# Kernel tuning notes

Hardware: AMD Instinct MI355X
Metric: run time of the kernel (lower is better)

Reference implementation:

```python
import jax, jax.numpy as jnp
import numpy as np

B, S = 8, 128
D_SENS, D_ACT, D_STR, D_ENC, DIM = 512, 32, 128, 128, 128
D_JOINT = D_STR + D_ENC  # 256


def _l2norm(x):
    return x / jnp.clip(jnp.linalg.norm(x, axis=-1, keepdims=True), 1e-12)


def _mlp(x, layers):
    # layers: list of (W, b); ReLU between layers, none on output
    n = len(layers)
    for i, (W, b) in enumerate(layers):
        x = x @ W + b
        if i < n - 1:
            x = jax.nn.relu(x)
    return x


def _meta_mlp(x, p):
    x = jax.nn.relu(x @ p['W1'] + p['b1'])
    x = jax.nn.relu(x @ p['W2'] + p['b2'])
    return x @ p['W3'] + p['b3']


def setup_inputs() -> dict:
    key = jax.random.key(0)
    it = iter(jax.random.split(key, 40))
    w = lambda shape, s=0.02: jax.random.normal(next(it), shape, jnp.float32) * s
    H = D_ACT * 4  # to_transitions hidden dim (default mlp_hidden_dim)
    return dict(
        sensory=jax.random.normal(next(it), (B, S, D_SENS), jnp.float32),
        actions=jax.random.normal(next(it), (B, S, D_ACT), jnp.float32),
        init_hidden=w((1, D_STR), 0.01),
        tW1=w((D_ACT, H)), tb1=w((H,)),
        tW2=w((H, H)), tb2=w((H,)),
        tW3=w((H, D_STR * D_STR)), tb3=w((D_STR * D_STR,)),
        enc_w=w((D_SENS, D_ENC)), enc_b=w((D_ENC,)),
        dec_w=w((D_ENC, D_SENS)), dec_b=w((D_SENS,)),
        q_w=w((D_JOINT, DIM)), k_w=w((D_JOINT, DIM)), v_w=w((D_JOINT, DIM)),
        mW1=w((DIM, 2 * DIM)), mb1=w((2 * DIM,)),
        mW2=w((2 * DIM, 2 * DIM)), mb2=w((2 * DIM,)),
        mW3=w((2 * DIM, DIM)), mb3=w((DIM,)),
        oW1=w((DIM, 2 * DIM)), ob1=w((2 * DIM,)),
        oW2=w((2 * DIM, 2 * DIM)), ob2=w((2 * DIM,)),
        oW3=w((2 * DIM, D_JOINT)), ob3=w((D_JOINT,)),
        sW1=w((2 * D_STR + 1, 2 * D_STR)), sb1=w((2 * D_STR,)),
        sW2=w((2 * D_STR, 2 * D_STR)), sb2=w((2 * D_STR,)),
        sW3=w((2 * D_STR, D_STR)), sb3=w((D_STR,)),
        integration_ratio=jnp.asarray(0.1, jnp.float32),
    )


def reference(sensory, actions, init_hidden, tW1, tb1, tW2, tb2, tW3, tb3,
              enc_w, enc_b, dec_w, dec_b, q_w, k_w, v_w,
              mW1, mb1, mW2, mb2, mW3, mb3,
              oW1, ob1, oW2, ob2, oW3, ob3,
              sW1, sb1, sW2, sb2, sW3, sb3, integration_ratio):
    mse = lambda a, b: jnp.mean((a - b) ** 2)

    # --- PathIntegration: actions -> transitions -> scripted RNN scan ---
    trans = _mlp(actions, [(tW1, tb1), (tW2, tb2), (tW3, tb3)])  # (B,S,ds*ds)
    trans = trans.reshape(B, S, D_STR, D_STR)
    h0 = jnp.broadcast_to(_l2norm(init_hidden), (B, D_STR))

    def step(h, T):  # h (B,ds), T (B,ds,ds)
        h = _l2norm(jax.nn.relu(jnp.einsum('bi,bij->bj', h, T)))
        return h, h

    _, hs = jax.lax.scan(step, h0, jnp.swapaxes(trans, 0, 1))
    structural = jnp.swapaxes(hs, 0, 1)  # (B,S,ds)

    # --- sensory encoder (Linear) ---
    encoded = sensory @ enc_w + enc_b  # (B,S,D_ENC)

    meta_params = {'W1': mW1, 'b1': mb1, 'W2': mW2, 'b2': mb2, 'W3': mW3, 'b3': mb3}

    def retrieve(s, e):
        joint = jnp.concatenate((s, e), axis=-1)
        q = joint @ q_w
        r = _meta_mlp(q, meta_params)
        out = _mlp(r, [(oW1, ob1), (oW2, ob2), (oW3, ob3)])
        return out[..., :D_STR], out[..., D_STR:]

    # generative branch
    dec_gen_s, dec_enc = retrieve(structural, jnp.zeros_like(encoded))
    generative_pred_loss = mse(sensory, dec_enc @ dec_w + dec_b)

    # relational branch (source calls retrieve(zeros, encoded) twice)
    dec_s1, _ = retrieve(jnp.zeros_like(structural), encoded)
    dec_s2, _ = retrieve(jnp.zeros_like(structural), encoded)
    relational_loss = mse(dec_s1, structural) + mse(dec_s2, structural)

    # consistency / inference correction
    corr_s, corr_e = retrieve(dec_gen_s, encoded)
    sse = jnp.sum((corr_e - encoded) ** 2, axis=-1, keepdims=True)  # (B,S,1)
    pred_var = _mlp(jnp.concatenate((corr_s, dec_gen_s, sse), axis=-1),
                    [(sW1, sb1), (sW2, sb2), (sW3, sb3)])
    inf_s = dec_gen_s + (corr_s - dec_gen_s) * integration_ratio * pred_var
    consistency_loss = mse(dec_gen_s, inf_s)

    final_s, inf_e = retrieve(inf_s, jnp.zeros_like(encoded))
    inference_pred_loss = mse(sensory, inf_e @ dec_w + dec_b)

    # per-sample fast-weight memory gradients (nested vmap(grad))
    store = jnp.concatenate((final_s, encoded), axis=-1)
    keys = store @ k_w
    values = store @ v_w

    def meta_loss(p, k, v):
        return jnp.mean((_meta_mlp(k, p) - v) ** 2)

    per_grad = jax.vmap(jax.vmap(jax.grad(meta_loss), in_axes=(None, 0, 0)),
                        in_axes=(None, 0, 0))
    g = per_grad(meta_params, keys, values)  # each leaf (B,S,*param_shape)

    total = (generative_pred_loss + relational_loss
             + consistency_loss + inference_pred_loss)  # all loss weights 1.0
    return (total, g['W1'], g['b1'], g['W2'], g['b2'], g['W3'], g['b3'])
```

## Files before the change

kernel.cpp:

```cpp
#include <hip/hip_runtime.h>
#include <hip/hip_bf16.h>

constexpr size_t OFF_W1 = 1;
constexpr size_t OFF_B1 = OFF_W1 + (size_t)1024*32768;
constexpr size_t OFF_W2 = OFF_B1 + (size_t)1024*256;
constexpr size_t OFF_B2 = OFF_W2 + (size_t)1024*65536;
constexpr size_t OFF_W3 = OFF_B2 + (size_t)1024*256;
constexpr size_t OFF_B3 = OFF_W3 + (size_t)1024*32768;

__device__ __forceinline__ void layer_n256_r8(
    const float* __restrict__ W, const float* __restrict__ bias, int K,
    const float* __restrict__ x, int xs, float* __restrict__ y, int relu, int t)
{
    const int c4 = (t & 63) * 4;
    const int r0 = (t >> 6) * 2;
    float4 a0 = bias ? *(const float4*)&bias[c4] : make_float4(0.f,0.f,0.f,0.f);
    float4 a1 = a0;
    const float* x0 = x + r0 * xs;
    const float* x1 = x0 + xs;
    for (int k = 0; k < K; ++k) {
        float4 w = *(const float4*)&W[(size_t)k*256 + c4];
        float xa = x0[k], xb = x1[k];
        a0.x = fmaf(w.x, xa, a0.x); a0.y = fmaf(w.y, xa, a0.y);
        a0.z = fmaf(w.z, xa, a0.z); a0.w = fmaf(w.w, xa, a0.w);
        a1.x = fmaf(w.x, xb, a1.x); a1.y = fmaf(w.y, xb, a1.y);
        a1.z = fmaf(w.z, xb, a1.z); a1.w = fmaf(w.w, xb, a1.w);
    }
    if (relu) {
        a0.x=fmaxf(a0.x,0.f); a0.y=fmaxf(a0.y,0.f); a0.z=fmaxf(a0.z,0.f); a0.w=fmaxf(a0.w,0.f);
        a1.x=fmaxf(a1.x,0.f); a1.y=fmaxf(a1.y,0.f); a1.z=fmaxf(a1.z,0.f); a1.w=fmaxf(a1.w,0.f);
    }
    *(float4*)&y[r0*256 + c4] = a0;
    *(float4*)&y[(r0+1)*256 + c4] = a1;
}

__device__ __forceinline__ void layer_n256_r4(
    const float* __restrict__ W, const float* __restrict__ bias, int K,
    const float* __restrict__ x, int xs, float* __restrict__ y, int relu,
    const float* __restrict__ mask, int t)
{
    const int c4 = (t & 63) * 4;
    const int r = t >> 6;
    float4 a = bias ? *(const float4*)&bias[c4] : make_float4(0.f,0.f,0.f,0.f);
    const float* xr = x + r * xs;
    for (int k = 0; k < K; ++k) {
        float4 w = *(const float4*)&W[(size_t)k*256 + c4];
        float xa = xr[k];
        a.x = fmaf(w.x, xa, a.x); a.y = fmaf(w.y, xa, a.y);
        a.z = fmaf(w.z, xa, a.z); a.w = fmaf(w.w, xa, a.w);
    }
    if (relu) {
        a.x=fmaxf(a.x,0.f); a.y=fmaxf(a.y,0.f); a.z=fmaxf(a.z,0.f); a.w=fmaxf(a.w,0.f);
    }
    if (mask) {
        float4 m = *(const float4*)&mask[r*256 + c4];
        a.x = (m.x > 0.f) ? a.x : 0.f; a.y = (m.y > 0.f) ? a.y : 0.f;
        a.z = (m.z > 0.f) ? a.z : 0.f; a.w = (m.w > 0.f) ? a.w : 0.f;
    }
    *(float4*)&y[r*256 + c4] = a;
}

__device__ __forceinline__ void layer_n128(
    const float* __restrict__ W, const float* __restrict__ bias, int K,
    const float* __restrict__ x, int xs, float* __restrict__ y, int ys, int relu,
    int rows, int t)
{
    const int c4 = (t & 31) * 4;
    int r = t >> 5; if (rows == 4) r &= 3;
    float4 a = bias ? *(const float4*)&bias[c4] : make_float4(0.f,0.f,0.f,0.f);
    const float* xr = x + r * xs;
    for (int k = 0; k < K; ++k) {
        float4 w = *(const float4*)&W[(size_t)k*128 + c4];
        float xa = xr[k];
        a.x = fmaf(w.x, xa, a.x); a.y = fmaf(w.y, xa, a.y);
        a.z = fmaf(w.z, xa, a.z); a.w = fmaf(w.w, xa, a.w);
    }
    if (relu) {
        a.x=fmaxf(a.x,0.f); a.y=fmaxf(a.y,0.f); a.z=fmaxf(a.z,0.f); a.w=fmaxf(a.w,0.f);
    }
    *(float4*)&y[r*ys + c4] = a;
}

__device__ __forceinline__ void layer_n128_dual(
    const float* __restrict__ W,
    const float* __restrict__ xA, const float* __restrict__ xB,
    float* __restrict__ y, int rows, int t)
{
    const int c4 = (t & 31) * 4;
    int r = t >> 5; if (rows == 4) r &= 3;
    float4 a = make_float4(0.f,0.f,0.f,0.f);
    const float* xa_ = xA + r * 128;
    const float* xb_ = xB + r * 128;
    for (int k = 0; k < 128; ++k) {
        float4 w = *(const float4*)&W[(size_t)k*128 + c4];
        float v = xa_[k];
        a.x = fmaf(w.x, v, a.x); a.y = fmaf(w.y, v, a.y);
        a.z = fmaf(w.z, v, a.z); a.w = fmaf(w.w, v, a.w);
    }
    for (int k = 0; k < 128; ++k) {
        float4 w = *(const float4*)&W[(size_t)(128+k)*128 + c4];
        float v = xb_[k];
        a.x = fmaf(w.x, v, a.x); a.y = fmaf(w.y, v, a.y);
        a.z = fmaf(w.z, v, a.z); a.w = fmaf(w.w, v, a.w);
    }
    *(float4*)&y[r*128 + c4] = a;
}

__device__ __forceinline__ void block_mse_commit(float s, float scale,
                                                 float* __restrict__ accum,
                                                 float* __restrict__ red, int t)
{
    #pragma unroll
    for (int off = 32; off > 0; off >>= 1) s += __shfl_down(s, off, 64);
    if ((t & 63) == 0) red[t >> 6] = s;
    __syncthreads();
    if (t == 0) atomicAdd(accum, (red[0]+red[1]+red[2]+red[3]) * scale);
}

__device__ __forceinline__ void dec_mse(
    const float* __restrict__ ret,
    const float* __restrict__ sensory, int row0,
    const float* __restrict__ dec_w, const float* __restrict__ dec_b,
    float* __restrict__ accum, float* __restrict__ red, int t)
{
    const int c4 = (t & 127) * 4;
    const int rb = (t >> 7) * 2;
    float4 a0 = *(const float4*)&dec_b[c4];
    float4 a1 = a0;
    const float* x0 = ret + rb*256 + 128;
    const float* x1 = x0 + 256;
    for (int k = 0; k < 128; ++k) {
        float4 w = *(const float4*)&dec_w[(size_t)k*512 + c4];
        float xa = x0[k], xb = x1[k];
        a0.x = fmaf(w.x, xa, a0.x); a0.y = fmaf(w.y, xa, a0.y);
        a0.z = fmaf(w.z, xa, a0.z); a0.w = fmaf(w.w, xa, a0.w);
        a1.x = fmaf(w.x, xb, a1.x); a1.y = fmaf(w.y, xb, a1.y);
        a1.z = fmaf(w.z, xb, a1.z); a1.w = fmaf(w.w, xb, a1.w);
    }
    float4 s0 = *(const float4*)&sensory[(size_t)(row0+rb)*512 + c4];
    float4 s1 = *(const float4*)&sensory[(size_t)(row0+rb+1)*512 + c4];
    float dx0 = a0.x-s0.x, dy0 = a0.y-s0.y, dz0 = a0.z-s0.z, dw0 = a0.w-s0.w;
    float dx1 = a1.x-s1.x, dy1 = a1.y-s1.y, dz1 = a1.z-s1.z, dw1 = a1.w-s1.w;
    float s = dx0*dx0 + dy0*dy0 + dz0*dz0 + dw0*dw0
            + dx1*dx1 + dy1*dy1 + dz1*dz1 + dw1*dw1;
    block_mse_commit(s, 1.f/524288.f, accum, red, t);
}

__global__ __launch_bounds__(256) void prep_kernel(
    const float* __restrict__ tW3,
    const float* __restrict__ mW2, const float* __restrict__ mW3,
    const float* __restrict__ actions,
    const float* __restrict__ tW1, const float* __restrict__ tb1,
    const float* __restrict__ tW2, const float* __restrict__ tb2,
    const float* __restrict__ sensory,
    const float* __restrict__ enc_w, const float* __restrict__ enc_b,
    float* __restrict__ tW3T, float* __restrict__ T2, float* __restrict__ T3,
    float* __restrict__ acc, float* __restrict__ a2, float* __restrict__ encoded)
{
    __shared__ float smem[64*129];
    const int t = threadIdx.x;
    const int bid = blockIdx.x;
    if (bid < 256) {
        const int k = bid >> 1, i0 = (bid & 1) * 64;
        const size_t base = (size_t)k << 14;
        for (int l = t; l < 8192; l += 256) {
            int ii = l >> 7, jj = l & 127;
            smem[ii*129 + jj] = tW3[base + (size_t)(i0+ii)*128 + jj];
        }
        __syncthreads();
        for (int l = t; l < 8192; l += 256) {
            int jj = l >> 6, ii = l & 63;
            tW3T[base + (size_t)jj*128 + i0 + ii] = smem[ii*129 + jj];
        }
    } else if (bid < 512) {
        const int c = bid - 256;
        T2[(size_t)c*256 + t] = mW2[(size_t)t*256 + c];
    } else if (bid < 640) {
        const int c = bid - 512;
        T3[(size_t)c*256 + t] = mW3[(size_t)t*128 + c];
    } else if (bid == 640) {
        if (t < 16) acc[t] = 0.f;
    } else if (bid < 769) {
        float* bufAct = smem;
        float* ping   = smem + 256;
        float* pong   = smem + 1280;
        const int row0 = (bid - 641) * 8;
        if (t < 64) {
            int r = t >> 3, c4 = (t & 7) * 4;
            *(float4*)&bufAct[r*32 + c4] =
                *(const float4*)&actions[(size_t)(row0 + r)*32 + c4];
        }
        __syncthreads();
        layer_n128(tW1, tb1, 32, bufAct, 32, ping, 128, 1, 8, t);
        __syncthreads();
        layer_n128(tW2, tb2, 128, ping, 128, pong, 128, 1, 8, t);
        __syncthreads();
        {
            int r = t >> 5, c4 = (t & 31) * 4;
            *(float4*)&a2[(size_t)(row0 + r)*128 + c4] = *(const float4*)&pong[r*128 + c4];
        }
    } else {
        const int q = bid - 769;
        const int m0 = (q & 15) * 64, n0 = (q >> 4) * 64;
        float (*As)[65] = (float(*)[65])smem;
        float (*Ws)[65] = (float(*)[65])(smem + 16*65);
        const int tx = t & 15, ty = t >> 4;
        float a4[4][4] = {};
        for (int k0 = 0; k0 < 512; k0 += 16) {
            for (int l = t; l < 1024; l += 256) {
                int mm = l >> 4, kk = l & 15;
                As[kk][mm] = sensory[(size_t)(m0+mm)*512 + k0 + kk];
            }
            for (int l = t; l < 1024; l += 256) {
                int kk = l >> 6, nn = l & 63;
                Ws[kk][nn] = enc_w[(size_t)(k0+kk)*128 + n0 + nn];
            }
            __syncthreads();
            #pragma unroll
            for (int kk = 0; kk < 16; ++kk) {
                float a[4], b[4];
                #pragma unroll
                for (int i=0;i<4;i++) a[i] = As[kk][ty*4+i];
                #pragma unroll
                for (int j=0;j<4;j++) b[j] = Ws[kk][tx*4+j];
                #pragma unroll
                for (int i=0;i<4;i++)
                    #pragma unroll
                    for (int j=0;j<4;j++)
                        a4[i][j] = fmaf(a[i], b[j], a4[i][j]);
            }
            __syncthreads();
        }
        #pragma unroll
        for (int i=0;i<4;i++){
            int gm = m0 + ty*4 + i;
            #pragma unroll
            for (int j=0;j<4;j++){
                int gn = n0 + tx*4 + j;
                encoded[(size_t)gm*128 + gn] = a4[i][j] + enc_b[gn];
            }
        }
    }
}

__global__ __launch_bounds__(256) void gemm_k128_kernel(
    const float* __restrict__ A, int lda, const float* __restrict__ W,
    const float* __restrict__ bias, float* __restrict__ C, int N)
{
    __shared__ float As[128*36];
    const int t = threadIdx.x;
    const int m0 = blockIdx.x * 32, n0 = blockIdx.y * 256;
    for (int l = t; l < 4096; l += 256) {
        int r = l >> 7, k = l & 127;
        As[k*36 + r] = A[(size_t)(m0 + r)*lda + k];
    }
    __syncthreads();
    const int c4 = (t & 63) * 4;
    const int r0 = (t >> 6) * 8;
    float4 bv;
    {
        const int n = n0 + c4;
        const int j = n >> 7, i = n & 127;
        bv.x = bias[(size_t)(i+0)*128 + j];
        bv.y = bias[(size_t)(i+1)*128 + j];
        bv.z = bias[(size_t)(i+2)*128 + j];
        bv.w = bias[(size_t)(i+3)*128 + j];
    }
    float4 acc[8];
    #pragma unroll
    for (int i = 0; i < 8; ++i) acc[i] = bv;
    const float* Wp = W + (size_t)n0 + c4;
    #pragma unroll 4
    for (int k = 0; k < 128; ++k) {
        float4 w = *(const float4*)&Wp[(size_t)k*N];
        float a[8];
        *(float4*)&a[0] = *(const float4*)&As[k*36 + r0];
        *(float4*)&a[4] = *(const float4*)&As[k*36 + r0 + 4];
        #pragma unroll
        for (int i = 0; i < 8; ++i) {
            acc[i].x = fmaf(w.x, a[i], acc[i].x);
            acc[i].y = fmaf(w.y, a[i], acc[i].y);
            acc[i].z = fmaf(w.z, a[i], acc[i].z);
            acc[i].w = fmaf(w.w, a[i], acc[i].w);
        }
    }
    #pragma unroll
    for (int i = 0; i < 8; ++i)
        *(float4*)&C[(size_t)(m0 + r0 + i)*N + n0 + c4] = acc[i];
}

__global__ __launch_bounds__(512) void scanrel_kernel(
    const float* __restrict__ transT,
    const float* __restrict__ init_hidden,
    float* __restrict__ structural,
    const float* __restrict__ encoded,
    const float* __restrict__ qw,
    const float* __restrict__ mW1, const float* __restrict__ mb1,
    const float* __restrict__ mW2, const float* __restrict__ mb2,
    const float* __restrict__ mW3, const float* __restrict__ mb3,
    const float* __restrict__ oW1, const float* __restrict__ ob1,
    const float* __restrict__ oW2, const float* __restrict__ ob2,
    const float* __restrict__ oW3, const float* __restrict__ ob3,
    float* __restrict__ out2)
{
    __shared__ float smem[5120];
    const int tid = threadIdx.x;
    if (blockIdx.x < 8) {
        float* h  = smem;
        float* ws = smem + 128;
        const int b = blockIdx.x;
        const int j = tid >> 2, p = tid & 3;
        const int i0 = p * 32;

        if (tid < 32) {
            float4 v = *(const float4*)&init_hidden[tid*4];
            float ss = v.x*v.x + v.y*v.y + v.z*v.z + v.w*v.w;
            ss += __shfl_xor(ss, 16); ss += __shfl_xor(ss, 8); ss += __shfl_xor(ss, 4);
            ss += __shfl_xor(ss, 2);  ss += __shfl_xor(ss, 1);
            float inv = 1.f / fmaxf(sqrtf(ss), 1e-12f);
            v.x *= inv; v.y *= inv; v.z *= inv; v.w *= inv;
            *(float4*)&h[tid*4] = v;
        }
        __syncthreads();

        const size_t bbase = ((size_t)b) << 21;
        const int lane_off = j*128 + i0;
        float4 cur[8], nxt[8];
        {
            const float* T0 = transT + bbase + lane_off;
            #pragma unroll
            for (int r = 0; r < 8; ++r) cur[r] = *(const float4*)&T0[r*4];
        }
        for (int t = 0; t < 128; ++t) {
            const int tn = (t < 127) ? t + 1 : 127;
            const float* Tn = transT + bbase + ((size_t)tn << 14) + lane_off;
            #pragma unroll
            for (int r = 0; r < 8; ++r) nxt[r] = *(const float4*)&Tn[r*4];

            float4 a = make_float4(0.f, 0.f, 0.f, 0.f);
            #pragma unroll
            for (int r = 0; r < 8; ++r) {
                float4 hv = *(const float4*)&h[i0 + r*4];
                a.x = fmaf(hv.x, cur[r].x, a.x);
                a.y = fmaf(hv.y, cur[r].y, a.y);
                a.z = fmaf(hv.z, cur[r].z, a.z);
                a.w = fmaf(hv.w, cur[r].w, a.w);
            }
            float s = (a.x + a.y) + (a.z + a.w);
            s += __shfl_xor(s, 1);
            s += __shfl_xor(s, 2);
            float v = fmaxf(s, 0.f);
            float q = v * v;
            q += __shfl_xor(q, 4);  q += __shfl_xor(q, 8);
            q += __shfl_xor(q, 16); q += __shfl_xor(q, 32);
            if ((tid & 63) == 0) ws[tid >> 6] = q;
            __syncthreads();
            float ss = ((ws[0]+ws[1]) + (ws[2]+ws[3])) + ((ws[4]+ws[5]) + (ws[6]+ws[7]));
            float inv = 1.f / fmaxf(sqrtf(ss), 1e-12f);
            float hv = v * inv;
            __syncthreads();
            if (p == 0) h[j] = hv;
            else if (p == 1) structural[(((size_t)(b*128 + t)) << 7) + j] = hv;
            __syncthreads();
            #pragma unroll
            for (int r = 0; r < 8; ++r) cur[r] = nxt[r];
        }
    } else {
        float* bufB = smem;
        float* ping = smem + 1024;
        float* pong = smem + 3072;
        const int row0 = (blockIdx.x - 8) * 8;
        const bool act = (tid < 256);
        const int t = tid;
        if (act) {
            int r = t >> 5, k4 = (t & 31) * 4;
            *(float4*)&bufB[r*128 + k4] =
                *(const float4*)&encoded[(size_t)(row0 + r)*128 + k4];
        }
        __syncthreads();
        if (act) layer_n128(qw + (size_t)128*128, nullptr, 128, bufB, 128, ping, 128, 0, 8, t);
        __syncthreads();
        if (act) layer_n256_r8(mW1, mb1, 128, ping, 128, pong, 1, t);
        __syncthreads();
        if (act) layer_n256_r8(mW2, mb2, 256, pong, 256, ping, 1, t);
        __syncthreads();
        if (act) layer_n128(mW3, mb3, 256, ping, 256, pong, 128, 0, 8, t);
        __syncthreads();
        if (act) layer_n256_r8(oW1, ob1, 128, pong, 128, ping, 1, t);
        __syncthreads();
        if (act) layer_n256_r8(oW2, ob2, 256, ping, 256, pong, 1, t);
        __syncthreads();
        if (act) layer_n256_r8(oW3, ob3, 256, pong, 256, ping, 0, t);
        __syncthreads();
        if (act) {
            for (int e = t; e < 512; e += 256) {
                int r = e >> 6, c = (e & 63) * 4;
                *(float4*)&out2[(size_t)(row0+r)*256 + c] = *(const float4*)&ping[r*256 + c];
            }
        }
    }
}

__global__ __launch_bounds__(256) void mega_kernel(
    const float* __restrict__ structural, const float* __restrict__ encoded,
    const float* __restrict__ out2, const float* __restrict__ sensory,
    const float* __restrict__ ratio_p,
    const float* __restrict__ qw,
    const float* __restrict__ mW1, const float* __restrict__ mb1,
    const float* __restrict__ mW2, const float* __restrict__ mb2,
    const float* __restrict__ mW3, const float* __restrict__ mb3,
    const float* __restrict__ oW1, const float* __restrict__ ob1,
    const float* __restrict__ oW2, const float* __restrict__ ob2,
    const float* __restrict__ oW3, const float* __restrict__ ob3,
    const float* __restrict__ sW1, const float* __restrict__ sb1,
    const float* __restrict__ sW2, const float* __restrict__ sb2,
    const float* __restrict__ sW3, const float* __restrict__ sb3,
    const float* __restrict__ k_w, const float* __restrict__ v_w,
    const float* __restrict__ T2, const float* __restrict__ T3,
    const float* __restrict__ dec_w, const float* __restrict__ dec_b,
    float* __restrict__ acc, float* __restrict__ out)
{
    __shared__ float smem[9736];
    float* enc_s    = smem;
    float* struct_s = smem + 512;
    float* ping     = smem + 1024;
    float* pong     = smem + 2048;
    float* ret1     = smem + 3072;
    float* xa128    = smem + 4096;
    float* out3_s   = smem + 4608;
    float* pvar_s   = smem + 5632;
    float* infs_s   = smem + 6144;
    float* ks       = smem + 6656;
    float* vs       = smem + 7168;
    float* h1       = smem + 7680;
    float* h2       = smem + 8704;
    float* sse      = smem + 9728;
    float* red      = smem + 9732;
    const int t = threadIdx.x;
    const int row0 = blockIdx.x * 4;

    {
        int r = (t >> 5) & 3, k4 = (t & 31) * 4;
        *(float4*)&struct_s[r*128 + k4] = *(const float4*)&structural[(size_t)(row0+r)*128 + k4];
        *(float4*)&enc_s[r*128 + k4]    = *(const float4*)&encoded[(size_t)(row0+r)*128 + k4];
    }
    __syncthreads();
    layer_n128(qw, nullptr, 128, struct_s, 128, ping, 128, 0, 4, t); __syncthreads();
    layer_n256_r4(mW1, mb1, 128, ping, 128, pong, 1, nullptr, t); __syncthreads();
    layer_n256_r4(mW2, mb2, 256, pong, 256, ping, 1, nullptr, t); __syncthreads();
    layer_n128(mW3, mb3, 256, ping, 256, pong, 128, 0, 4, t); __syncthreads();
    layer_n256_r4(oW1, ob1, 128, pong, 128, ping, 1, nullptr, t); __syncthreads();
    layer_n256_r4(oW2, ob2, 256, ping, 256, pong, 1, nullptr, t); __syncthreads();
    layer_n256_r4(oW3, ob3, 256, pong, 256, ret1, 0, nullptr, t); __syncthreads();
    {
        float relsum = 0.f;
        for (int e = t; e < 512; e += 256) {
            int r = e >> 7, c = e & 127;
            xa128[e] = ret1[r*256 + c];
            float d = out2[(size_t)(row0+r)*256 + c] - struct_s[r*128 + c];
            relsum = fmaf(d, d, relsum);
        }
        block_mse_commit(relsum, 2.f/131072.f, acc + 1, red, t);
    }
    __syncthreads();
    dec_mse(ret1, sensory, row0, dec_w, dec_b, acc + 0, red, t);
    __syncthreads();
    layer_n128_dual(qw, xa128, enc_s, ping, 4, t); __syncthreads();
    layer_n256_r4(mW1, mb1, 128, ping, 128, pong, 1, nullptr, t); __syncthreads();
    layer_n256_r4(mW2, mb2, 256, pong, 256, ping, 1, nullptr, t); __syncthreads();
    layer_n128(mW3, mb3, 256, ping, 256, pong, 128, 0, 4, t); __syncthreads();
    layer_n256_r4(oW1, ob1, 128, pong, 128, ping, 1, nullptr, t); __syncthreads();
    layer_n256_r4(oW2, ob2, 256, ping, 256, pong, 1, nullptr, t); __syncthreads();
    layer_n256_r4(oW3, ob3, 256, pong, 256, out3_s, 0, nullptr, t); __syncthreads();
    {
        int r = (t >> 5) & 3, k4 = (t & 31) * 4;
        float4 ce = *(const float4*)&out3_s[r*256 + 128 + k4];
        float4 en = *(const float4*)&enc_s[r*128 + k4];
        float dx = ce.x-en.x, dy = ce.y-en.y, dz = ce.z-en.z, dw = ce.w-en.w;
        float ss = dx*dx + dy*dy + dz*dz + dw*dw;
        ss += __shfl_xor(ss, 16); ss += __shfl_xor(ss, 8); ss += __shfl_xor(ss, 4);
        ss += __shfl_xor(ss, 2);  ss += __shfl_xor(ss, 1);
        if ((t & 31) == 0) sse[r] = ss;
    }
    __syncthreads();
    {
        const int c4 = (t & 63) * 4;
        const int r = t >> 6;
        float4 a = *(const float4*)&sb1[c4];
        for (int k = 0; k < 128; ++k) {
            float4 w = *(const float4*)&sW1[(size_t)k*256 + c4];
            float xa = out3_s[r*256 + k];
            a.x=fmaf(w.x,xa,a.x); a.y=fmaf(w.y,xa,a.y); a.z=fmaf(w.z,xa,a.z); a.w=fmaf(w.w,xa,a.w);
        }
        for (int k = 0; k < 128; ++k) {
            float4 w = *(const float4*)&sW1[(size_t)(128+k)*256 + c4];
            float xa = xa128[r*128 + k];
            a.x=fmaf(w.x,xa,a.x); a.y=fmaf(w.y,xa,a.y); a.z=fmaf(w.z,xa,a.z); a.w=fmaf(w.w,xa,a.w);
        }
        {
            float4 w = *(const float4*)&sW1[(size_t)256*256 + c4];
            float xa = sse[r];
            a.x=fmaf(w.x,xa,a.x); a.y=fmaf(w.y,xa,a.y); a.z=fmaf(w.z,xa,a.z); a.w=fmaf(w.w,xa,a.w);
        }
        a.x=fmaxf(a.x,0.f); a.y=fmaxf(a.y,0.f); a.z=fmaxf(a.z,0.f); a.w=fmaxf(a.w,0.f);
        *(float4*)&ping[r*256 + c4] = a;
    }
    __syncthreads();
    layer_n256_r4(sW2, sb2, 256, ping, 256, pong, 1, nullptr, t); __syncthreads();
    layer_n128(sW3, sb3, 256, pong, 256, pvar_s, 128, 0, 4, t); __syncthreads();
    {
        float ratio = ratio_p[0];
        float ssum = 0.f;
        for (int e = t; e < 512; e += 256) {
            int r = e >> 7, j = e & 127;
            float dgs = xa128[r*128 + j];
            float cs  = out3_s[r*256 + j];
            float pv  = pvar_s[r*128 + j];
            float delta = (cs - dgs) * ratio * pv;
            infs_s[r*128 + j] = dgs + delta;
            ssum = fmaf(delta, delta, ssum);
        }
        block_mse_commit(ssum, 1.f/131072.f, acc + 2, red, t);
    }
    __syncthreads();
    layer_n128(qw, nullptr, 128, infs_s, 128, ping, 128, 0, 4, t); __syncthreads();
    layer_n256_r4(mW1, mb1, 128, ping, 128, pong, 1, nullptr, t); __syncthreads();
    layer_n256_r4(mW2, mb2, 256, pong, 256, ping, 1, nullptr, t); __syncthreads();
    layer_n128(mW3, mb3, 256, ping, 256, pong, 128, 0, 4, t); __syncthreads();
    layer_n256_r4(oW1, ob1, 128, pong, 128, ping, 1, nullptr, t); __syncthreads();
    layer_n256_r4(oW2, ob2, 256, ping, 256, pong, 1, nullptr, t); __syncthreads();
    layer_n256_r4(oW3, ob3, 256, pong, 256, ret1, 0, nullptr, t); __syncthreads();
    dec_mse(ret1, sensory, row0, dec_w, dec_b, acc + 3, red, t);
    __syncthreads();
    for (int e = t; e < 512; e += 256) {
        int r = e >> 7, c = e & 127;
        xa128[e] = ret1[r*256 + c];
    }
    __syncthreads();
    float* dob = pvar_s;
    float* dh2 = out3_s;
    float* dh1 = ping;
    layer_n128_dual(k_w, xa128, enc_s, ks, 4, t);
    layer_n128_dual(v_w, xa128, enc_s, vs, 4, t);
    __syncthreads();
    layer_n256_r4(mW1, mb1, 128, ks, 128, h1, 1, nullptr, t);
    __syncthreads();
    layer_n256_r4(mW2, mb2, 256, h1, 256, h2, 1, nullptr, t);
    __syncthreads();
    layer_n128(mW3, mb3, 256, h2, 256, dob, 128, 0, 4, t);
    __syncthreads();
    for (int e = t; e < 512; e += 256)
        dob[e] = (dob[e] - vs[e]) * 0.015625f;
    __syncthreads();
    layer_n256_r4(T3, nullptr, 128, dob, 128, dh2, 0, h2, t);
    __syncthreads();
    layer_n256_r4(T2, nullptr, 256, dh2, 256, dh1, 0, h1, t);
    __syncthreads();
    #pragma unroll
    for (int r = 0; r < 4; ++r) {
        const size_t row = row0 + r;
        {
            const int c4 = (t & 63) * 4;
            const int i0 = (t >> 6) * 32;
            const float4 dv = *(const float4*)&dh1[r*256 + c4];
            float* p = out + OFF_W1 + row*32768;
            for (int i = i0; i < i0 + 32; ++i) {
                float kv = ks[r*128 + i];
                float4 o; o.x = kv*dv.x; o.y = kv*dv.y; o.z = kv*dv.z; o.w = kv*dv.w;
                *(float4*)&p[(size_t)i*256 + c4] = o;
            }
            out[OFF_B1 + row*256 + t] = dh1[r*256 + t];
        }
        {
            const int c4 = (t & 63) * 4;
            const int i0 = (t >> 6) * 64;
            const float4 dv = *(const float4*)&dh2[r*256 + c4];
            float* p = out + OFF_W2 + row*65536;
            for (int i = i0; i < i0 + 64; ++i) {
                float hv = h1[r*256 + i];
                float4 o; o.x = hv*dv.x; o.y = hv*dv.y; o.z = hv*dv.z; o.w = hv*dv.w;
                *(float4*)&p[(size_t)i*256 + c4] = o;
            }
            out[OFF_B2 + row*256 + t] = dh2[r*256 + t];
        }
        {
            const int c4 = (t & 31) * 4;
            const int i0 = (t >> 5) * 32;
            const float4 dv = *(const float4*)&dob[r*128 + c4];
            float* p = out + OFF_W3 + row*32768;
            for (int i = i0; i < i0 + 32; ++i) {
                float hv = h2[r*256 + i];
                float4 o; o.x = hv*dv.x; o.y = hv*dv.y; o.z = hv*dv.z; o.w = hv*dv.w;
                *(float4*)&p[(size_t)i*128 + c4] = o;
            }
            if (t < 128) out[OFF_B3 + row*128 + t] = dob[r*128 + t];
        }
    }
}

__global__ void total_kernel(const float* acc, float* out) {
    if (threadIdx.x == 0)
        out[0] = acc[0] + acc[1] + acc[2] + acc[3];
}

extern "C" void kernel_launch(void* const* d_in, const int* in_sizes, int n_in,
                              void* d_out, int out_size, void* d_ws, size_t ws_size,
                              hipStream_t stream)
{
    const float* sensory     = (const float*)d_in[0];
    const float* actions     = (const float*)d_in[1];
    const float* init_hidden = (const float*)d_in[2];
    const float* tW1 = (const float*)d_in[3];  const float* tb1 = (const float*)d_in[4];
    const float* tW2 = (const float*)d_in[5];  const float* tb2 = (const float*)d_in[6];
    const float* tW3 = (const float*)d_in[7];  const float* tb3 = (const float*)d_in[8];
    const float* enc_w = (const float*)d_in[9];  const float* enc_b = (const float*)d_in[10];
    const float* dec_w = (const float*)d_in[11]; const float* dec_b = (const float*)d_in[12];
    const float* q_w = (const float*)d_in[13];
    const float* k_w = (const float*)d_in[14];
    const float* v_w = (const float*)d_in[15];
    const float* mW1 = (const float*)d_in[16]; const float* mb1 = (const float*)d_in[17];
    const float* mW2 = (const float*)d_in[18]; const float* mb2 = (const float*)d_in[19];
    const float* mW3 = (const float*)d_in[20]; const float* mb3 = (const float*)d_in[21];
    const float* oW1 = (const float*)d_in[22]; const float* ob1 = (const float*)d_in[23];
    const float* oW2 = (const float*)d_in[24]; const float* ob2 = (const float*)d_in[25];
    const float* oW3 = (const float*)d_in[26]; const float* ob3 = (const float*)d_in[27];
    const float* sW1 = (const float*)d_in[28]; const float* sb1 = (const float*)d_in[29];
    const float* sW2 = (const float*)d_in[30]; const float* sb2 = (const float*)d_in[31];
    const float* sW3 = (const float*)d_in[32]; const float* sb3 = (const float*)d_in[33];
    const float* ratio = (const float*)d_in[34];
    float* out = (float*)d_out;

    float* Wsp = (float*)d_ws;
    float* acc   = Wsp;
    float* ALIAS = Wsp + 16;
    float* structural = ALIAS + 131072;
    float* out2 = ALIAS + 524288;
    float* tW3T = ALIAS;
    size_t off = 16 + 2097152;
    float* a2      = Wsp + off; off += 131072;
    float* encoded = Wsp + off; off += 131072;
    float* transT  = Wsp + off; off += 16777216;
    float* T2      = Wsp + off; off += 65536;
    float* T3      = Wsp + off; off += 32768;

    prep_kernel<<<801, 256, 0, stream>>>(tW3, mW2, mW3, actions, tW1, tb1, tW2, tb2,
                                         sensory, enc_w, enc_b, tW3T, T2, T3,
                                         acc, a2, encoded);

    gemm_k128_kernel<<<dim3(32, 64), 256, 0, stream>>>(a2, 128, tW3T, tb3, transT, 16384);

    scanrel_kernel<<<136, 512, 0, stream>>>(transT, init_hidden, structural, encoded,
        q_w, mW1, mb1, mW2, mb2, mW3, mb3, oW1, ob1, oW2, ob2, oW3, ob3, out2);

    mega_kernel<<<256, 256, 0, stream>>>(structural, encoded, out2, sensory, ratio,
        q_w, mW1, mb1, mW2, mb2, mW3, mb3, oW1, ob1, oW2, ob2, oW3, ob3,
        sW1, sb1, sW2, sb2, sW3, sb3, k_w, v_w, T2, T3, dec_w, dec_b, acc, out);

    total_kernel<<<1, 64, 0, stream>>>(acc, out);
}
```

Baseline: 1.321 ms.

## Halve rows per block in mega kernel and use all 512 threads in scanrel MLP

The mega kernel now processes 2 rows per block instead of 4 and launches 512 blocks, with each thread computing fewer output columns (float2 or scalar instead of float4). This spreads the per-row MLP chain across more CUs, since 256 blocks underfill the device. In the relational part of scanrel_kernel, all 512 threads now run the 256-wide layers instead of only 256 threads. The cost is that each weight matrix is re-read from cache by twice as many blocks, and loads are narrower.

```diff
diff --git a/kernel.cpp b/kernel.cpp
--- a/kernel.cpp
+++ b/kernel.cpp
@@ -8,36 +8,30 @@
 constexpr size_t OFF_W3 = OFF_B2 + (size_t)1024*256;
 constexpr size_t OFF_B3 = OFF_W3 + (size_t)1024*32768;
 
-__device__ __forceinline__ void layer_n256_r8(
+__device__ __forceinline__ void layer_n128(
+    const float* __restrict__ W, const float* __restrict__ bias, int K,
+    const float* __restrict__ x, int xs, float* __restrict__ y, int ys, int relu,
+    int rows, int t)
+{
+    const int c4 = (t & 31) * 4;
+    int r = t >> 5; if (rows == 4) r &= 3;
+    float4 a = bias ? *(const float4*)&bias[c4] : make_float4(0.f,0.f,0.f,0.f);
+    const float* xr = x + r * xs;
+    for (int k = 0; k < K; ++k) {
+        float4 w = *(const float4*)&W[(size_t)k*128 + c4];
+        float xa = xr[k];
+        a.x = fmaf(w.x, xa, a.x); a.y = fmaf(w.y, xa, a.y);
+        a.z = fmaf(w.z, xa, a.z); a.w = fmaf(w.w, xa, a.w);
+    }
+    if (relu) {
+        a.x=fmaxf(a.x,0.f); a.y=fmaxf(a.y,0.f); a.z=fmaxf(a.z,0.f); a.w=fmaxf(a.w,0.f);
+    }
+    *(float4*)&y[r*ys + c4] = a;
+}
+
+__device__ __forceinline__ void layer_n256_512(
     const float* __restrict__ W, const float* __restrict__ bias, int K,
     const float* __restrict__ x, int xs, float* __restrict__ y, int relu, int t)
-{
-    const int c4 = (t & 63) * 4;
-    const int r0 = (t >> 6) * 2;
-    float4 a0 = bias ? *(const float4*)&bias[c4] : make_float4(0.f,0.f,0.f,0.f);
-    float4 a1 = a0;
-    const float* x0 = x + r0 * xs;
-    const float* x1 = x0 + xs;
-    for (int k = 0; k < K; ++k) {
-        float4 w = *(const float4*)&W[(size_t)k*256 + c4];
-        float xa = x0[k], xb = x1[k];
-        a0.x = fmaf(w.x, xa, a0.x); a0.y = fmaf(w.y, xa, a0.y);
-        a0.z = fmaf(w.z, xa, a0.z); a0.w = fmaf(w.w, xa, a0.w);
-        a1.x = fmaf(w.x, xb, a1.x); a1.y = fmaf(w.y, xb, a1.y);
-        a1.z = fmaf(w.z, xb, a1.z); a1.w = fmaf(w.w, xb, a1.w);
-    }
-    if (relu) {
-        a0.x=fmaxf(a0.x,0.f); a0.y=fmaxf(a0.y,0.f); a0.z=fmaxf(a0.z,0.f); a0.w=fmaxf(a0.w,0.f);
-        a1.x=fmaxf(a1.x,0.f); a1.y=fmaxf(a1.y,0.f); a1.z=fmaxf(a1.z,0.f); a1.w=fmaxf(a1.w,0.f);
-    }
-    *(float4*)&y[r0*256 + c4] = a0;
-    *(float4*)&y[(r0+1)*256 + c4] = a1;
-}
-
-__device__ __forceinline__ void layer_n256_r4(
-    const float* __restrict__ W, const float* __restrict__ bias, int K,
-    const float* __restrict__ x, int xs, float* __restrict__ y, int relu,
-    const float* __restrict__ mask, int t)
 {
     const int c4 = (t & 63) * 4;
     const int r = t >> 6;
@@ -52,58 +46,56 @@
     if (relu) {
         a.x=fmaxf(a.x,0.f); a.y=fmaxf(a.y,0.f); a.z=fmaxf(a.z,0.f); a.w=fmaxf(a.w,0.f);
     }
-    if (mask) {
-        float4 m = *(const float4*)&mask[r*256 + c4];
-        a.x = (m.x > 0.f) ? a.x : 0.f; a.y = (m.y > 0.f) ? a.y : 0.f;
-        a.z = (m.z > 0.f) ? a.z : 0.f; a.w = (m.w > 0.f) ? a.w : 0.f;
-    }
     *(float4*)&y[r*256 + c4] = a;
 }
 
-__device__ __forceinline__ void layer_n128(
+__device__ __forceinline__ void layer2_n256(
     const float* __restrict__ W, const float* __restrict__ bias, int K,
-    const float* __restrict__ x, int xs, float* __restrict__ y, int ys, int relu,
-    int rows, int t)
-{
-    const int c4 = (t & 31) * 4;
-    int r = t >> 5; if (rows == 4) r &= 3;
-    float4 a = bias ? *(const float4*)&bias[c4] : make_float4(0.f,0.f,0.f,0.f);
+    const float* __restrict__ x, int xs, float* __restrict__ y, int relu,
+    const float* __restrict__ mask, int t)
+{
+    const int r = t >> 7;
+    const int c2 = (t & 127) * 2;
+    float2 a = bias ? *(const float2*)&bias[c2] : make_float2(0.f, 0.f);
     const float* xr = x + r * xs;
     for (int k = 0; k < K; ++k) {
-        float4 w = *(const float4*)&W[(size_t)k*128 + c4];
+        float2 w = *(const float2*)&W[(size_t)k*256 + c2];
         float xa = xr[k];
         a.x = fmaf(w.x, xa, a.x); a.y = fmaf(w.y, xa, a.y);
-        a.z = fmaf(w.z, xa, a.z); a.w = fmaf(w.w, xa, a.w);
-    }
-    if (relu) {
-        a.x=fmaxf(a.x,0.f); a.y=fmaxf(a.y,0.f); a.z=fmaxf(a.z,0.f); a.w=fmaxf(a.w,0.f);
-    }
-    *(float4*)&y[r*ys + c4] = a;
-}
-
-__device__ __forceinline__ void layer_n128_dual(
+    }
+    if (relu) { a.x = fmaxf(a.x, 0.f); a.y = fmaxf(a.y, 0.f); }
+    if (mask) {
+        float2 m = *(const float2*)&mask[r*256 + c2];
+        a.x = (m.x > 0.f) ? a.x : 0.f; a.y = (m.y > 0.f) ? a.y : 0.f;
+    }
+    *(float2*)&y[r*256 + c2] = a;
+}
+
+__device__ __forceinline__ void layer2_n128(
+    const float* __restrict__ W, const float* __restrict__ bias, int K,
+    const float* __restrict__ x, int xs, float* __restrict__ y, int ys, int relu, int t)
+{
+    const int r = t >> 7, c = t & 127;
+    float a = bias ? bias[c] : 0.f;
+    const float* xr = x + r * xs;
+    for (int k = 0; k < K; ++k)
+        a = fmaf(W[(size_t)k*128 + c], xr[k], a);
+    if (relu) a = fmaxf(a, 0.f);
+    y[r*ys + c] = a;
+}
+
+__device__ __forceinline__ void layer2_n128_dual(
     const float* __restrict__ W,
     const float* __restrict__ xA, const float* __restrict__ xB,
-    float* __restrict__ y, int rows, int t)
-{
-    const int c4 = (t & 31) * 4;
-    int r = t >> 5; if (rows == 4) r &= 3;
-    float4 a = make_float4(0.f,0.f,0.f,0.f);
+    float* __restrict__ y, int t)
+{
+    const int r = t >> 7, c = t & 127;
+    float a = 0.f;
     const float* xa_ = xA + r * 128;
     const float* xb_ = xB + r * 128;
-    for (int k = 0; k < 128; ++k) {
-        float4 w = *(const float4*)&W[(size_t)k*128 + c4];
-        float v = xa_[k];
-        a.x = fmaf(w.x, v, a.x); a.y = fmaf(w.y, v, a.y);
-        a.z = fmaf(w.z, v, a.z); a.w = fmaf(w.w, v, a.w);
-    }
-    for (int k = 0; k < 128; ++k) {
-        float4 w = *(const float4*)&W[(size_t)(128+k)*128 + c4];
-        float v = xb_[k];
-        a.x = fmaf(w.x, v, a.x); a.y = fmaf(w.y, v, a.y);
-        a.z = fmaf(w.z, v, a.z); a.w = fmaf(w.w, v, a.w);
-    }
-    *(float4*)&y[r*128 + c4] = a;
+    for (int k = 0; k < 128; ++k) a = fmaf(W[(size_t)k*128 + c], xa_[k], a);
+    for (int k = 0; k < 128; ++k) a = fmaf(W[(size_t)(128+k)*128 + c], xb_[k], a);
+    y[r*128 + c] = a;
 }
 
 __device__ __forceinline__ void block_mse_commit(float s, float scale,
@@ -117,32 +109,25 @@
     if (t == 0) atomicAdd(accum, (red[0]+red[1]+red[2]+red[3]) * scale);
 }
 
-__device__ __forceinline__ void dec_mse(
+__device__ __forceinline__ void dec_mse2(
     const float* __restrict__ ret,
     const float* __restrict__ sensory, int row0,
     const float* __restrict__ dec_w, const float* __restrict__ dec_b,
     float* __restrict__ accum, float* __restrict__ red, int t)
 {
     const int c4 = (t & 127) * 4;
-    const int rb = (t >> 7) * 2;
-    float4 a0 = *(const float4*)&dec_b[c4];
-    float4 a1 = a0;
+    const int rb = t >> 7;
+    float4 a = *(const float4*)&dec_b[c4];
     const float* x0 = ret + rb*256 + 128;
-    const float* x1 = x0 + 256;
     for (int k = 0; k < 128; ++k) {
         float4 w = *(const float4*)&dec_w[(size_t)k*512 + c4];
-        float xa = x0[k], xb = x1[k];
-        a0.x = fmaf(w.x, xa, a0.x); a0.y = fmaf(w.y, xa, a0.y);
-        a0.z = fmaf(w.z, xa, a0.z); a0.w = fmaf(w.w, xa, a0.w);
-        a1.x = fmaf(w.x, xb, a1.x); a1.y = fmaf(w.y, xb, a1.y);
-        a1.z = fmaf(w.z, xb, a1.z); a1.w = fmaf(w.w, xb, a1.w);
+        float xa = x0[k];
+        a.x = fmaf(w.x, xa, a.x); a.y = fmaf(w.y, xa, a.y);
+        a.z = fmaf(w.z, xa, a.z); a.w = fmaf(w.w, xa, a.w);
     }
     float4 s0 = *(const float4*)&sensory[(size_t)(row0+rb)*512 + c4];
-    float4 s1 = *(const float4*)&sensory[(size_t)(row0+rb+1)*512 + c4];
-    float dx0 = a0.x-s0.x, dy0 = a0.y-s0.y, dz0 = a0.z-s0.z, dw0 = a0.w-s0.w;
-    float dx1 = a1.x-s1.x, dy1 = a1.y-s1.y, dz1 = a1.z-s1.z, dw1 = a1.w-s1.w;
-    float s = dx0*dx0 + dy0*dy0 + dz0*dz0 + dw0*dw0
-            + dx1*dx1 + dy1*dy1 + dz1*dz1 + dw1*dw1;
+    float dx = a.x-s0.x, dy = a.y-s0.y, dz = a.z-s0.z, dw = a.w-s0.w;
+    float s = dx*dx + dy*dy + dz*dz + dw*dw;
     block_mse_commit(s, 1.f/524288.f, accum, red, t);
 }
 
@@ -370,33 +355,30 @@
         float* ping = smem + 1024;
         float* pong = smem + 3072;
         const int row0 = (blockIdx.x - 8) * 8;
-        const bool act = (tid < 256);
         const int t = tid;
-        if (act) {
+        if (t < 256) {
             int r = t >> 5, k4 = (t & 31) * 4;
             *(float4*)&bufB[r*128 + k4] =
                 *(const float4*)&encoded[(size_t)(row0 + r)*128 + k4];
         }
         __syncthreads();
-        if (act) layer_n128(qw + (size_t)128*128, nullptr, 128, bufB, 128, ping, 128, 0, 8, t);
-        __syncthreads();
-        if (act) layer_n256_r8(mW1, mb1, 128, ping, 128, pong, 1, t);
-        __syncthreads();
-        if (act) layer_n256_r8(mW2, mb2, 256, pong, 256, ping, 1, t);
-        __syncthreads();
-        if (act) layer_n128(mW3, mb3, 256, ping, 256, pong, 128, 0, 8, t);
-        __syncthreads();
-        if (act) layer_n256_r8(oW1, ob1, 128, pong, 128, ping, 1, t);
-        __syncthreads();
-        if (act) layer_n256_r8(oW2, ob2, 256, ping, 256, pong, 1, t);
-        __syncthreads();
-        if (act) layer_n256_r8(oW3, ob3, 256, pong, 256, ping, 0, t);
-        __syncthreads();
-        if (act) {
-            for (int e = t; e < 512; e += 256) {
-                int r = e >> 6, c = (e & 63) * 4;
-                *(float4*)&out2[(size_t)(row0+r)*256 + c] = *(const float4*)&ping[r*256 + c];
-            }
+        if (t < 256) layer_n128(qw + (size_t)128*128, nullptr, 128, bufB, 128, ping, 128, 0, 8, t);
+        __syncthreads();
+        layer_n256_512(mW1, mb1, 128, ping, 128, pong, 1, t);
+        __syncthreads();
+        layer_n256_512(mW2, mb2, 256, pong, 256, ping, 1, t);
+        __syncthreads();
+        if (t < 256) layer_n128(mW3, mb3, 256, ping, 256, pong, 128, 0, 8, t);
+        __syncthreads();
+        layer_n256_512(oW1, ob1, 128, pong, 128, ping, 1, t);
+        __syncthreads();
+        layer_n256_512(oW2, ob2, 256, ping, 256, pong, 1, t);
+        __syncthreads();
+        layer_n256_512(oW3, ob3, 256, pong, 256, ping, 0, t);
+        __syncthreads();
+        {
+            int r = t >> 6, c = (t & 63) * 4;
+            *(float4*)&out2[(size_t)(row0+r)*256 + c] = *(const float4*)&ping[r*256 + c];
         }
     }
 }
@@ -420,144 +402,130 @@
     const float* __restrict__ dec_w, const float* __restrict__ dec_b,
     float* __restrict__ acc, float* __restrict__ out)
 {
-    __shared__ float smem[9736];
+    __shared__ float smem[4880];
     float* enc_s    = smem;
-    float* struct_s = smem + 512;
-    float* ping     = smem + 1024;
-    float* pong     = smem + 2048;
-    float* ret1     = smem + 3072;
-    float* xa128    = smem + 4096;
-    float* out3_s   = smem + 4608;
-    float* pvar_s   = smem + 5632;
-    float* infs_s   = smem + 6144;
-    float* ks       = smem + 6656;
-    float* vs       = smem + 7168;
-    float* h1       = smem + 7680;
-    float* h2       = smem + 8704;
-    float* sse      = smem + 9728;
-    float* red      = smem + 9732;
+    float* struct_s = smem + 256;
+    float* ping     = smem + 512;
+    float* pong     = smem + 1024;
+    float* ret1     = smem + 1536;
+    float* xa128    = smem + 2048;
+    float* out3_s   = smem + 2304;
+    float* pvar_s   = smem + 2816;
+    float* infs_s   = smem + 3072;
+    float* ks       = smem + 3328;
+    float* vs       = smem + 3584;
+    float* h1       = smem + 3840;
+    float* h2       = smem + 4352;
+    float* sse      = smem + 4864;
+    float* wsse     = smem + 4866;
+    float* red      = smem + 4872;
     const int t = threadIdx.x;
-    const int row0 = blockIdx.x * 4;
-
+    const int row0 = blockIdx.x * 2;
+    const int tr = t >> 7, tc = t & 127;
+
+    if (t < 64) {
+        int r = t >> 5, k4 = (t & 31) * 4;
+        *(float4*)&struct_s[r*128 + k4] = *(const float4*)&structural[(size_t)(row0+r)*128 + k4];
+    } else if (t < 128) {
+        int tt = t - 64;
+        int r = tt >> 5, k4 = (tt & 31) * 4;
+        *(float4*)&enc_s[r*128 + k4] = *(const float4*)&encoded[(size_t)(row0+r)*128 + k4];
+    }
+    __syncthreads();
+    layer2_n128(qw, nullptr, 128, struct_s, 128, ping, 128, 0, t); __syncthreads();
+    layer2_n256(mW1, mb1, 128, ping, 128, pong, 1, nullptr, t); __syncthreads();
+    layer2_n256(mW2, mb2, 256, pong, 256, ping, 1, nullptr, t); __syncthreads();
+    layer2_n128(mW3, mb3, 256, ping, 256, pong, 128, 0, t); __syncthreads();
+    layer2_n256(oW1, ob1, 128, pong, 128, ping, 1, nullptr, t); __syncthreads();
+    layer2_n256(oW2, ob2, 256, ping, 256, pong, 1, nullptr, t); __syncthreads();
+    layer2_n256(oW3, ob3, 256, pong, 256, ret1, 0, nullptr, t); __syncthreads();
     {
-        int r = (t >> 5) & 3, k4 = (t & 31) * 4;
-        *(float4*)&struct_s[r*128 + k4] = *(const float4*)&structural[(size_t)(row0+r)*128 + k4];
-        *(float4*)&enc_s[r*128 + k4]    = *(const float4*)&encoded[(size_t)(row0+r)*128 + k4];
-    }
-    __syncthreads();
-    layer_n128(qw, nullptr, 128, struct_s, 128, ping, 128, 0, 4, t); __syncthreads();
-    layer_n256_r4(mW1, mb1, 128, ping, 128, pong, 1, nullptr, t); __syncthreads();
-    layer_n256_r4(mW2, mb2, 256, pong, 256, ping, 1, nullptr, t); __syncthreads();
-    layer_n128(mW3, mb3, 256, ping, 256, pong, 128, 0, 4, t); __syncthreads();
-    layer_n256_r4(oW1, ob1, 128, pong, 128, ping, 1, nullptr, t); __syncthreads();
-    layer_n256_r4(oW2, ob2, 256, ping, 256, pong, 1, nullptr, t); __syncthreads();
-    layer_n256_r4(oW3, ob3, 256, pong, 256, ret1, 0, nullptr, t); __syncthreads();
+        xa128[t] = ret1[tr*256 + tc];
+        float d = out2[(size_t)(row0+tr)*256 + tc] - struct_s[t];
+        block_mse_commit(d * d, 2.f/131072.f, acc + 1, red, t);
+    }
+    __syncthreads();
+    dec_mse2(ret1, sensory, row0, dec_w, dec_b, acc + 0, red, t);
+    __syncthreads();
+    layer2_n128_dual(qw, xa128, enc_s, ping, t); __syncthreads();
+    layer2_n256(mW1, mb1, 128, ping, 128, pong, 1, nullptr, t); __syncthreads();
+    layer2_n256(mW2, mb2, 256, pong, 256, ping, 1, nullptr, t); __syncthreads();
+    layer2_n128(mW3, mb3, 256, ping, 256, pong, 128, 0, t); __syncthreads();
+    layer2_n256(oW1, ob1, 128, pong, 128, ping, 1, nullptr, t); __syncthreads();
+    layer2_n256(oW2, ob2, 256, ping, 256, pong, 1, nullptr, t); __syncthreads();
+    layer2_n256(oW3, ob3, 256, pong, 256, out3_s, 0, nullptr, t); __syncthreads();
     {
-        float relsum = 0.f;
-        for (int e = t; e < 512; e += 256) {
-            int r = e >> 7, c = e & 127;
-            xa128[e] = ret1[r*256 + c];
-            float d = out2[(size_t)(row0+r)*256 + c] - struct_s[r*128 + c];
-            relsum = fmaf(d, d, relsum);
-        }
-        block_mse_commit(relsum, 2.f/131072.f, acc + 1, red, t);
-    }
-    __syncthreads();
-    dec_mse(ret1, sensory, row0, dec_w, dec_b, acc + 0, red, t);
-    __syncthreads();
-    layer_n128_dual(qw, xa128, enc_s, ping, 4, t); __syncthreads();
-    layer_n256_r4(mW1, mb1, 128, ping, 128, pong, 1, nullptr, t); __syncthreads();
-    layer_n256_r4(mW2, mb2, 256, pong, 256, ping, 1, nullptr, t); __syncthreads();
-    layer_n128(mW3, mb3, 256, ping, 256, pong, 128, 0, 4, t); __syncthreads();
-    layer_n256_r4(oW1, ob1, 128, pong, 128, ping, 1, nullptr, t); __syncthreads();
-    layer_n256_r4(oW2, ob2, 256, ping, 256, pong, 1, nullptr, t); __syncthreads();
-    layer_n256_r4(oW3, ob3, 256, pong, 256, out3_s, 0, nullptr, t); __syncthreads();
+        float ce = out3_s[tr*256 + 128 + tc];
+        float en = enc_s[t];
+        float d = ce - en;
+        float s = d * d;
+        #pragma unroll
+        for (int off = 32; off > 0; off >>= 1) s += __shfl_down(s, off, 64);
+        if ((t & 63) == 0) wsse[t >> 6] = s;
+    }
+    __syncthreads();
+    if (t < 2) sse[t] = wsse[2*t] + wsse[2*t + 1];
+    __syncthreads();
     {
-        int r = (t >> 5) & 3, k4 = (t & 31) * 4;
-        float4 ce = *(const float4*)&out3_s[r*256 + 128 + k4];
-        float4 en = *(const float4*)&enc_s[r*128 + k4];
-        float dx = ce.x-en.x, dy = ce.y-en.y, dz = ce.z-en.z, dw = ce.w-en.w;
-        float ss = dx*dx + dy*dy + dz*dz + dw*dw;
-        ss += __shfl_xor(ss, 16); ss += __shfl_xor(ss, 8); ss += __shfl_xor(ss, 4);
-        ss += __shfl_xor(ss, 2);  ss += __shfl_xor(ss, 1);
-        if ((t & 31) == 0) sse[r] = ss;
-    }
-    __syncthreads();
-    {
-        const int c4 = (t & 63) * 4;
-        const int r = t >> 6;
-        float4 a = *(const float4*)&sb1[c4];
+        const int r = t >> 7, c2 = (t & 127) * 2;
+        float2 a = *(const float2*)&sb1[c2];
         for (int k = 0; k < 128; ++k) {
-            float4 w = *(const float4*)&sW1[(size_t)k*256 + c4];
+            float2 w = *(const float2*)&sW1[(size_t)k*256 + c2];
             float xa = out3_s[r*256 + k];
-            a.x=fmaf(w.x,xa,a.x); a.y=fmaf(w.y,xa,a.y); a.z=fmaf(w.z,xa,a.z); a.w=fmaf(w.w,xa,a.w);
+            a.x = fmaf(w.x, xa, a.x); a.y = fmaf(w.y, xa, a.y);
         }
         for (int k = 0; k < 128; ++k) {
-            float4 w = *(const float4*)&sW1[(size_t)(128+k)*256 + c4];
+            float2 w = *(const float2*)&sW1[(size_t)(128+k)*256 + c2];
             float xa = xa128[r*128 + k];
-            a.x=fmaf(w.x,xa,a.x); a.y=fmaf(w.y,xa,a.y); a.z=fmaf(w.z,xa,a.z); a.w=fmaf(w.w,xa,a.w);
+            a.x = fmaf(w.x, xa, a.x); a.y = fmaf(w.y, xa, a.y);
         }
         {
-            float4 w = *(const float4*)&sW1[(size_t)256*256 + c4];
+            float2 w = *(const float2*)&sW1[(size_t)256*256 + c2];
             float xa = sse[r];
-            a.x=fmaf(w.x,xa,a.x); a.y=fmaf(w.y,xa,a.y); a.z=fmaf(w.z,xa,a.z); a.w=fmaf(w.w,xa,a.w);
-        }
-        a.x=fmaxf(a.x,0.f); a.y=fmaxf(a.y,0.f); a.z=fmaxf(a.z,0.f); a.w=fmaxf(a.w,0.f);
-        *(float4*)&ping[r*256 + c4] = a;
-    }
-    __syncthreads();
-    layer_n256_r4(sW2, sb2, 256, ping, 256, pong, 1, nullptr, t); __syncthreads();
-    layer_n128(sW3, sb3, 256, pong, 256, pvar_s, 128, 0, 4, t); __syncthreads();
+            a.x = fmaf(w.x, xa, a.x); a.y = fmaf(w.y, xa, a.y);
+        }
+        a.x = fmaxf(a.x, 0.f); a.y = fmaxf(a.y, 0.f);
+        *(float2*)&ping[r*256 + c2] = a;
+    }
+    __syncthreads();
+    layer2_n256(sW2, sb2, 256, ping, 256, pong, 1, nullptr, t); __syncthreads();
+    layer2_n128(sW3, sb3, 256, pong, 256, pvar_s, 128, 0, t); __syncthreads();
     {
         float ratio = ratio_p[0];
-        float ssum = 0.f;
-        for (int e = t; e < 512; e += 256) {
-            int r = e >> 7, j = e & 127;
-            float dgs = xa128[r*128 + j];
-            float cs  = out3_s[r*256 + j];
-            float pv  = pvar_s[r*128 + j];
-            float delta = (cs - dgs) * ratio * pv;
-            infs_s[r*128 + j] = dgs + delta;
-            ssum = fmaf(delta, delta, ssum);
-        }
-        block_mse_commit(ssum, 1.f/131072.f, acc + 2, red, t);
-    }
-    __syncthreads();
-    layer_n128(qw, nullptr, 128, infs_s, 128, ping, 128, 0, 4, t); __syncthreads();
-    layer_n256_r4(mW1, mb1, 128, ping, 128, pong, 1, nullptr, t); __syncthreads();
-    layer_n256_r4(mW2, mb2, 256, pong, 256, ping, 1, nullptr, t); __syncthreads();
-    layer_n128(mW3, mb3, 256, ping, 256, pong, 128, 0, 4, t); __syncthreads();
-    layer_n256_r4(oW1, ob1, 128, pong, 128, ping, 1, nullptr, t); __syncthreads();
-    layer_n256_r4(oW2, ob2, 256, ping, 256, pong, 1, nullptr, t); __syncthreads();
-    layer_n256_r4(oW3, ob3, 256, pong, 256, ret1, 0, nullptr, t); __syncthreads();
-    dec_mse(ret1, sensory, row0, dec_w, dec_b, acc + 3, red, t);
-    __syncthreads();
-    for (int e = t; e < 512; e += 256) {
-        int r = e >> 7, c = e & 127;
-        xa128[e] = ret1[r*256 + c];
-    }
+        float dgs = xa128[t];
+        float cs  = out3_s[tr*256 + tc];
+        float pv  = pvar_s[t];
+        float delta = (cs - dgs) * ratio * pv;
+        infs_s[t] = dgs + delta;
+        block_mse_commit(delta * delta, 1.f/131072.f, acc + 2, red, t);
+    }
+    __syncthreads();
+    layer2_n128(qw, nullptr, 128, infs_s, 128, ping, 128, 0, t); __syncthreads();
+    layer2_n256(mW1, mb1, 128, ping, 128, pong, 1, nullptr, t); __syncthreads();
+    layer2_n256(mW2, mb2, 256, pong, 256, ping, 1, nullptr, t); __syncthreads();
+    layer2_n128(mW3, mb3, 256, ping, 256, pong, 128, 0, t); __syncthreads();
+    layer2_n256(oW1, ob1, 128, pong, 128, ping, 1, nullptr, t); __syncthreads();
+    layer2_n256(oW2, ob2, 256, ping, 256, pong, 1, nullptr, t); __syncthreads();
+    layer2_n256(oW3, ob3, 256, pong, 256, ret1, 0, nullptr, t); __syncthreads();
+    dec_mse2(ret1, sensory, row0, dec_w, dec_b, acc + 3, red, t);
+    __syncthreads();
+    xa128[t] = ret1[tr*256 + tc];
     __syncthreads();
     float* dob = pvar_s;
     float* dh2 = out3_s;
     float* dh1 = ping;
-    layer_n128_dual(k_w, xa128, enc_s, ks, 4, t);
-    layer_n128_dual(v_w, xa128, enc_s, vs, 4, t);
-    __syncthreads();
-    layer_n256_r4(mW1, mb1, 128, ks, 128, h1, 1, nullptr, t);
-    __syncthreads();
-    layer_n256_r4(mW2, mb2, 256, h1, 256, h2, 1, nullptr, t);
-    __syncthreads();
-    layer_n128(mW3, mb3, 256, h2, 256, dob, 128, 0, 4, t);
-    __syncthreads();
-    for (int e = t; e < 512; e += 256)
-        dob[e] = (dob[e] - vs[e]) * 0.015625f;
-    __syncthreads();
-    layer_n256_r4(T3, nullptr, 128, dob, 128, dh2, 0, h2, t);
-    __syncthreads();
-    layer_n256_r4(T2, nullptr, 256, dh2, 256, dh1, 0, h1, t);
-    __syncthreads();
+    layer2_n128_dual(k_w, xa128, enc_s, ks, t);
+    layer2_n128_dual(v_w, xa128, enc_s, vs, t);
+    __syncthreads();
+    layer2_n256(mW1, mb1, 128, ks, 128, h1, 1, nullptr, t); __syncthreads();
+    layer2_n256(mW2, mb2, 256, h1, 256, h2, 1, nullptr, t); __syncthreads();
+    layer2_n128(mW3, mb3, 256, h2, 256, dob, 128, 0, t); __syncthreads();
+    dob[t] = (dob[t] - vs[t]) * 0.015625f;
+    __syncthreads();
+    layer2_n256(T3, nullptr, 128, dob, 128, dh2, 0, h2, t); __syncthreads();
+    layer2_n256(T2, nullptr, 256, dh2, 256, dh1, 0, h1, t); __syncthreads();
     #pragma unroll
-    for (int r = 0; r < 4; ++r) {
+    for (int r = 0; r < 2; ++r) {
         const size_t row = row0 + r;
         {
             const int c4 = (t & 63) * 4;
@@ -652,7 +620,7 @@
     scanrel_kernel<<<136, 512, 0, stream>>>(transT, init_hidden, structural, encoded,
         q_w, mW1, mb1, mW2, mb2, mW3, mb3, oW1, ob1, oW2, ob2, oW3, ob3, out2);
 
-    mega_kernel<<<256, 256, 0, stream>>>(structural, encoded, out2, sensory, ratio,
+    mega_kernel<<<512, 256, 0, stream>>>(structural, encoded, out2, sensory, ratio,
         q_w, mW1, mb1, mW2, mb2, mW3, mb3, oW1, ob1, oW2, ob2, oW3, ob3,
         sW1, sb1, sW2, sb2, sW3, sb3, k_w, v_w, T2, T3, dec_w, dec_b, acc, out);
 
```

After: 1.452 ms. +9.9%, slower.
